# Kernel optimization log

Hardware: AMD Instinct MI355X
Metric: run time of the kernel (lower is better)

The kernel has to match this reference:

```python
import jax, jax.numpy as jnp
import numpy as np

N = 100_000      # nodes
E = 3_200_000    # edges (avg degree 32)
IN = 128         # input feature dim
H1, C1 = 8, 8    # layer-1 heads, channels per head (concat -> 64)
OUT = 2          # output classes (layer-2: 1 head, mean/no-concat)
NEG = 0.2        # LeakyReLU negative slope (PyG default)


def setup_inputs() -> dict:
    key = jax.random.key(0)
    ks = jax.random.split(key, 11)
    s1 = 1.0 / np.sqrt(IN)
    s2 = 1.0 / np.sqrt(H1 * C1)
    return {
        "x": jax.random.normal(ks[0], (N, IN), jnp.float32),
        "edge_index": jax.random.randint(ks[1], (2, E), 0, N, dtype=jnp.int32),
        "edge_attr": jax.random.normal(ks[2], (E, 1), jnp.float32),
        "W1": jax.random.normal(ks[3], (IN, H1 * C1), jnp.float32) * s1,
        "a1_src": jax.random.normal(ks[4], (H1, C1), jnp.float32) * s1,
        "a1_dst": jax.random.normal(ks[5], (H1, C1), jnp.float32) * s1,
        "b1": jnp.zeros((H1 * C1,), jnp.float32),
        "W2": jax.random.normal(ks[6], (H1 * C1, OUT), jnp.float32) * s2,
        "a2_src": jax.random.normal(ks[7], (1, OUT), jnp.float32) * s2,
        "a2_dst": jax.random.normal(ks[8], (1, OUT), jnp.float32) * s2,
        "b2": jnp.zeros((OUT,), jnp.float32),
    }


def gat_conv(x, W, a_src, a_dst, b, src, dst, heads, ch, concat):
    """PyG GATConv: per-head linear, per-edge LeakyReLU attention, segment softmax over dst."""
    n = x.shape[0]
    h = (x @ W).reshape(n, heads, ch)                 # [N, H, C]
    al_src = jnp.sum(h * a_src, axis=-1)              # [N, H]
    al_dst = jnp.sum(h * a_dst, axis=-1)              # [N, H]
    e = al_src[src] + al_dst[dst]                     # [Etot, H]
    e = jnp.where(e > 0, e, NEG * e)                  # LeakyReLU
    m = jax.lax.stop_gradient(jax.ops.segment_max(e, dst, num_segments=n))
    ex = jnp.exp(e - m[dst])
    den = jax.ops.segment_sum(ex, dst, num_segments=n)
    alpha = ex / den[dst]                             # segment softmax
    out = jax.ops.segment_sum(alpha[:, :, None] * h[src], dst, num_segments=n)  # [N, H, C]
    out = out.reshape(n, heads * ch) if concat else out.mean(axis=1)
    return out + b


def reference(x, edge_index, edge_attr, W1, a1_src, a1_dst, b1, W2, a2_src, a2_dst, b2):
    # add_self_loops=True (PyG default)
    loops = jnp.arange(x.shape[0], dtype=edge_index.dtype)
    src = jnp.concatenate([edge_index[0], loops])
    dst = jnp.concatenate([edge_index[1], loops])
    h = gat_conv(x, W1, a1_src, a1_dst, b1, src, dst, H1, C1, True)
    h = jax.nn.elu(h)
    return gat_conv(h, W2, a2_src, a2_dst, b2, src, dst, 1, OUT, False)
```

## Files before the change

kernel.cpp:

```cpp
#include <hip/hip_runtime.h>
#include <math.h>

#define NNODES 100000
#define NEDGES 3200000
#define ETOT   (NEDGES + NNODES)
#define IN_DIM 128
#define NH1    8
#define NC1    8
#define HC     64
#define OUTC   2
#define NEGSL  0.2f
#define L2E    1.44269504f

#define NBUCK 391
#define EPB   4096
#define NBLK  782
#define TOTC  (NBUCK * NBLK)


__global__ __launch_bounds__(256) void histA(const int* __restrict__ ei,
                                             int* __restrict__ carr) {
    __shared__ int lh[NBUCK];
    int tid = threadIdx.x;
    for (int i = tid; i < NBUCK; i += 256) lh[i] = 0;
    __syncthreads();
    const int* dptr = ei + NEDGES;
    int base = blockIdx.x * EPB;
#pragma unroll
    for (int i = 0; i < EPB / 1024; i++) {
        int idx = base + i * 1024 + tid * 4;
        if (idx < NEDGES) {
            int4 d4 = *(const int4*)&dptr[idx];
            atomicAdd(&lh[d4.x >> 8], 1);
            atomicAdd(&lh[d4.y >> 8], 1);
            atomicAdd(&lh[d4.z >> 8], 1);
            atomicAdd(&lh[d4.w >> 8], 1);
        }
    }
    __syncthreads();
    for (int i = tid; i < NBUCK; i += 256)
        carr[i * NBLK + blockIdx.x] = lh[i];
}

__global__ __launch_bounds__(256) void scanA(int* __restrict__ carr,
                                             int* __restrict__ bsums) {
    int gid = blockIdx.x * 256 + threadIdx.x;
    int v = (gid < TOTC) ? carr[gid] : 0;
    int lane = threadIdx.x & 63, w = threadIdx.x >> 6;
    int x = v;
    for (int off = 1; off < 64; off <<= 1) {
        int y = __shfl_up(x, off, 64);
        if (lane >= off) x += y;
    }
    __shared__ int wt[4];
    if (lane == 63) wt[w] = x;
    __syncthreads();
    int add = 0;
    for (int i = 0; i < w; i++) add += wt[i];
    int incl = x + add;
    if (gid < TOTC) carr[gid] = incl - v;
    if (threadIdx.x == 255) bsums[blockIdx.x] = incl;
}

__global__ __launch_bounds__(1024) void scanB(int* __restrict__ bsums, int nb) {
    int tid = threadIdx.x;
    int base = tid * 4;
    int v[4]; int tot = 0;
#pragma unroll
    for (int j = 0; j < 4; j++) {
        v[j] = (base + j < nb) ? bsums[base + j] : 0;
        tot += v[j];
    }
    int lane = tid & 63, w = tid >> 6;
    int x = tot;
    for (int off = 1; off < 64; off <<= 1) {
        int y = __shfl_up(x, off, 64);
        if (lane >= off) x += y;
    }
    __shared__ int wt[16];
    if (lane == 63) wt[w] = x;
    __syncthreads();
    int add = 0;
    for (int i = 0; i < w; i++) add += wt[i];
    int pre = x + add - tot;
#pragma unroll
    for (int j = 0; j < 4; j++) {
        if (base + j < nb) bsums[base + j] = pre;
        pre += v[j];
    }
}

__global__ __launch_bounds__(256) void scanC(int* __restrict__ carr,
                                             const int* __restrict__ bsums) {
    int gid = blockIdx.x * 256 + threadIdx.x;
    if (gid < TOTC) carr[gid] += bsums[gid >> 8];
}

__global__ __launch_bounds__(256) void scatC(const int* __restrict__ ei,
                                             const int* __restrict__ soff,
                                             int* __restrict__ ebuf) {
    __shared__ int soffL[NBUCK];
    __shared__ int lh[NBUCK];
    int tid = threadIdx.x;
    for (int i = tid; i < NBUCK; i += 256) {
        soffL[i] = soff[i * NBLK + blockIdx.x];
        lh[i] = 0;
    }
    __syncthreads();
    int base = blockIdx.x * EPB;
#pragma unroll
    for (int i = 0; i < EPB / 1024; i++) {
        int idx = base + i * 1024 + tid * 4;
        if (idx < NEDGES) {
            int4 s4 = *(const int4*)&ei[idx];
            int4 d4 = *(const int4*)&ei[NEDGES + idx];
            int b0 = d4.x >> 8, b1 = d4.y >> 8, b2 = d4.z >> 8, b3 = d4.w >> 8;
            int r0 = atomicAdd(&lh[b0], 1);
            int r1 = atomicAdd(&lh[b1], 1);
            int r2 = atomicAdd(&lh[b2], 1);
            int r3 = atomicAdd(&lh[b3], 1);
            ebuf[soffL[b0] + r0] = s4.x | ((d4.x & 255) << 17);
            ebuf[soffL[b1] + r1] = s4.y | ((d4.y & 255) << 17);
            ebuf[soffL[b2] + r2] = s4.z | ((d4.z & 255) << 17);
            ebuf[soffL[b3] + r3] = s4.w | ((d4.w & 255) << 17);
        }
    }
}

__global__ __launch_bounds__(256) void buildD(const int* __restrict__ soff,
                                              const int* __restrict__ ebuf,
                                              int* __restrict__ rowoff,
                                              int* __restrict__ srcs) {
    int b = blockIdx.x, tid = threadIdx.x;
    int nb = min(256, NNODES - b * 256);
    int ebeg = soff[b * NBLK];
    int eend = (b == NBUCK - 1) ? NEDGES : soff[(b + 1) * NBLK];
    __shared__ int cnt2[256];
    __shared__ int rowL[256];
    __shared__ int wsum[4];
    cnt2[tid] = 0;
    __syncthreads();
    for (int e = ebeg + tid; e < eend; e += 256)
        atomicAdd(&cnt2[(ebuf[e] >> 17) & 255], 1);
    __syncthreads();
    int v = (tid < nb) ? cnt2[tid] + 1 : 0;
    int lane = tid & 63, w = tid >> 6;
    int x = v;
    for (int off = 1; off < 64; off <<= 1) {
        int y = __shfl_up(x, off, 64);
        if (lane >= off) x += y;
    }
    if (lane == 63) wsum[w] = x;
    __syncthreads();
    int add = 0;
    for (int i = 0; i < w; i++) add += wsum[i];
    int fbase = ebeg + b * 256;
    int row = fbase + x + add - v;
    if (tid < nb) {
        rowL[tid] = row;
        int gnode = b * 256 + tid;
        rowoff[gnode] = row;
        srcs[row + cnt2[tid]] = gnode;
        if (gnode == NNODES - 1) rowoff[NNODES] = ETOT;
    }
    __syncthreads();
    cnt2[tid] = 0;
    __syncthreads();
    for (int e = ebeg + tid; e < eend; e += 256) {
        int wv = ebuf[e];
        int dl = (wv >> 17) & 255;
        int r = atomicAdd(&cnt2[dl], 1);
        srcs[rowL[dl] + r] = wv & 0x1FFFF;
    }
}


__global__ __launch_bounds__(256) void gemm1(const float* __restrict__ x,
                                             const float* __restrict__ W1,
                                             const float* __restrict__ a1s,
                                             const float* __restrict__ a1d,
                                             unsigned short* __restrict__ h1b,
                                             float2* __restrict__ alE,
                                             float* __restrict__ al1d) {
    __shared__ float sW[IN_DIM * HC];
    int tid = threadIdx.x;
    const float4* W4 = (const float4*)W1;
    float4* sW4 = (float4*)sW;
#pragma unroll
    for (int i = 0; i < 8; i++)
        sW4[tid + i * 256] = W4[tid + i * 256];
    __syncthreads();

    int w = __builtin_amdgcn_readfirstlane(tid >> 6);
    int lane = tid & 63;
    int node0 = blockIdx.x * 16 + w * 4;
    const float* xr = x + (size_t)node0 * IN_DIM;

    float acc0 = 0.f, acc1 = 0.f, acc2 = 0.f, acc3 = 0.f;
#pragma unroll 8
    for (int k = 0; k < IN_DIM; k++) {
        float wv = sW[k * HC + lane];
        acc0 = fmaf(xr[k], wv, acc0);
        acc1 = fmaf(xr[IN_DIM + k], wv, acc1);
        acc2 = fmaf(xr[2 * IN_DIM + k], wv, acc2);
        acc3 = fmaf(xr[3 * IN_DIM + k], wv, acc3);
    }

    float accs[4] = {acc0, acc1, acc2, acc3};
    int head = lane >> 3, c = lane & 7;
    float as = a1s[head * NC1 + c], adv = a1d[head * NC1 + c];
#pragma unroll
    for (int n = 0; n < 4; n++) {
        int node = node0 + n;
        unsigned int u = __float_as_uint(accs[n]);
        h1b[node * HC + lane] =
            (unsigned short)((u + 0x7FFF + ((u >> 16) & 1)) >> 16);
        float ps = accs[n] * as;
        float pd = accs[n] * adv;
        for (int off = 1; off < 8; off <<= 1) {
            ps += __shfl_xor(ps, off, 64);
            pd += __shfl_xor(pd, off, 64);
        }
        if (c == 0) {
            alE[node * NH1 + head] = make_float2(exp2f(ps * L2E),
                                                 exp2f(ps * (NEGSL * L2E)));
            al1d[node * NH1 + head] = pd;
        }
    }
}


__global__ __launch_bounds__(256) void agg1(const unsigned short* __restrict__ h1b,
                                            const float2* __restrict__ alE,
                                            const float* __restrict__ al1d,
                                            const float* __restrict__ b1,
                                            const float* __restrict__ W2,
                                            const float* __restrict__ a2s,
                                            const float* __restrict__ a2d,
                                            const int* __restrict__ rowoff,
                                            const int* __restrict__ srcs,
                                            float4* __restrict__ nd2,
                                            float* __restrict__ al2d) {
    int w = threadIdx.x >> 6, lane = threadIdx.x & 63;
    int node = blockIdx.x * 4 + w;
    int q = lane & 15;
    float ald = al1d[node * NH1 + (q & 7)];
    float E1d = exp2f(ald * L2E);
    float E2d = exp2f(ald * (NEGSL * L2E));
    int beg = __builtin_amdgcn_readfirstlane(rowoff[node]);
    int end = __builtin_amdgcn_readfirstlane(rowoff[node + 1]);
    int pidx = (lane & 0x30) | (q >> 1);

    float den = 0.f, a0 = 0.f, a1 = 0.f, a2 = 0.f, a3 = 0.f;
    for (int base = beg; base < end; base += 64) {
        int idx = base + lane;
        int sv = srcs[idx < end ? idx : end - 1];
        int nq = min(16, (end - base + 3) >> 2);
        for (int t = 0; t < nq; t++) {
            int s = __shfl(sv, 4 * t + (lane >> 4), 64);
            float p = 0.f;
            if (q < 8) {
                float2 ea = alE[s * NH1 + q];
                p = fmaxf(ea.x * E1d, ea.y * E2d);
            }
            p = __shfl(p, pidx, 64);
            bool valid = (base + 4 * t + (lane >> 4)) < end;
            p = valid ? p : 0.f;
            uint2 hv = *(const uint2*)&h1b[s * HC + 4 * q];
            den += p;
            a0 = fmaf(p, __uint_as_float(hv.x << 16), a0);
            a1 = fmaf(p, __uint_as_float(hv.x & 0xFFFF0000u), a1);
            a2 = fmaf(p, __uint_as_float(hv.y << 16), a2);
            a3 = fmaf(p, __uint_as_float(hv.y & 0xFFFF0000u), a3);
        }
    }
    den += __shfl_xor(den, 16, 64);  den += __shfl_xor(den, 32, 64);
    a0  += __shfl_xor(a0, 16, 64);   a0  += __shfl_xor(a0, 32, 64);
    a1  += __shfl_xor(a1, 16, 64);   a1  += __shfl_xor(a1, 32, 64);
    a2  += __shfl_xor(a2, 16, 64);   a2  += __shfl_xor(a2, 32, 64);
    a3  += __shfl_xor(a3, 16, 64);   a3  += __shfl_xor(a3, 32, 64);

    float rd = 1.f / den;
    float4 b1v = *(const float4*)&b1[4 * q];
    float o0 = fmaf(a0, rd, b1v.x);
    float o1 = fmaf(a1, rd, b1v.y);
    float o2 = fmaf(a2, rd, b1v.z);
    float o3 = fmaf(a3, rd, b1v.w);
    o0 = (o0 > 0.f) ? o0 : expm1f(o0);
    o1 = (o1 > 0.f) ? o1 : expm1f(o1);
    o2 = (o2 > 0.f) ? o2 : expm1f(o2);
    o3 = (o3 > 0.f) ? o3 : expm1f(o3);
    float4 w2a = *(const float4*)&W2[8 * q];
    float4 w2b = *(const float4*)&W2[8 * q + 4];
    float p0 = o0 * w2a.x + o1 * w2a.z + o2 * w2b.x + o3 * w2b.z;
    float p1 = o0 * w2a.y + o1 * w2a.w + o2 * w2b.y + o3 * w2b.w;
    for (int off = 1; off < 16; off <<= 1) {
        p0 += __shfl_xor(p0, off, 64);
        p1 += __shfl_xor(p1, off, 64);
    }
    if (lane == 0) {
        float l2s = p0 * a2s[0] + p1 * a2s[1];
        float l2d = p0 * a2d[0] + p1 * a2d[1];
        nd2[node] = make_float4(exp2f(l2s * L2E), exp2f(l2s * (NEGSL * L2E)),
                                p0, p1);
        al2d[node] = l2d;
    }
}


__global__ __launch_bounds__(256) void agg2(const float4* __restrict__ nd2,
                                            const float* __restrict__ al2d,
                                            const float* __restrict__ b2,
                                            const int* __restrict__ rowoff,
                                            const int* __restrict__ srcs,
                                            float* __restrict__ out) {
    int w = threadIdx.x >> 6, lane = threadIdx.x & 63;
    int n = blockIdx.x * 4 + w;
    if (n >= NNODES) return;
    float ald = al2d[n];
    float E1d = exp2f(ald * L2E);
    float E2d = exp2f(ald * (NEGSL * L2E));
    int beg = rowoff[n], end = rowoff[n + 1];
    float den = 0.f, a0 = 0.f, a1 = 0.f;
    for (int idx = beg + lane; idx < end; idx += 64) {
        int s = srcs[idx];
        float4 nd = nd2[s];
        float p = fmaxf(nd.x * E1d, nd.y * E2d);
        den += p;
        a0 = fmaf(p, nd.z, a0);
        a1 = fmaf(p, nd.w, a1);
    }
    for (int off = 1; off < 64; off <<= 1) {
        den += __shfl_xor(den, off, 64);
        a0  += __shfl_xor(a0, off, 64);
        a1  += __shfl_xor(a1, off, 64);
    }
    if (lane == 0) {
        out[n * 2 + 0] = a0 / den + b2[0];
        out[n * 2 + 1] = a1 / den + b2[1];
    }
}


extern "C" void kernel_launch(void* const* d_in, const int* in_sizes, int n_in,
                              void* d_out, int out_size, void* d_ws, size_t ws_size,
                              hipStream_t stream) {
    const float* x   = (const float*)d_in[0];
    const int*   ei  = (const int*)  d_in[1];
    const float* W1  = (const float*)d_in[3];
    const float* a1s = (const float*)d_in[4];
    const float* a1d = (const float*)d_in[5];
    const float* b1  = (const float*)d_in[6];
    const float* W2  = (const float*)d_in[7];
    const float* a2s = (const float*)d_in[8];
    const float* a2d = (const float*)d_in[9];
    const float* b2  = (const float*)d_in[10];
    float* out = (float*)d_out;

    char* ws = (char*)d_ws;
    unsigned short* h1b = (unsigned short*)ws;
    float2* alE   = (float2*)(ws + (size_t)NNODES * HC * 2);
    float* al1d_  = (float*)(alE + (size_t)NNODES * NH1);
    float4* nd2   = (float4*)(al1d_ + (size_t)NNODES * NH1);
    float* al2d_  = (float*)(nd2 + NNODES);
    int* rowoff   = (int*)(al2d_ + NNODES);
    int* srcs     = rowoff + NNODES + 1;
    int* ebuf     = (int*)ws;
    int* carr     = ebuf + NEDGES;
    int* bsums    = carr + TOTC;

    const int NB_SC  = (TOTC + 255) / 256;
    const int NB_N4  = (NNODES + 3) / 4;
    const int NB_G   = NNODES / 16;

    histA<<<NBLK, 256, 0, stream>>>(ei, carr);
    scanA<<<NB_SC, 256, 0, stream>>>(carr, bsums);
    scanB<<<1, 1024, 0, stream>>>(bsums, NB_SC);
    scanC<<<NB_SC, 256, 0, stream>>>(carr, bsums);
    scatC<<<NBLK, 256, 0, stream>>>(ei, carr, ebuf);
    buildD<<<NBUCK, 256, 0, stream>>>(carr, ebuf, rowoff, srcs);

    gemm1<<<NB_G, 256, 0, stream>>>(x, W1, a1s, a1d, h1b, alE, al1d_);

    agg1<<<NB_N4, 256, 0, stream>>>(h1b, alE, al1d_, b1, W2, a2s, a2d,
                                    rowoff, srcs, nd2, al2d_);

    agg2<<<NB_N4, 256, 0, stream>>>(nd2, al2d_, b2, rowoff, srcs, out);
}
```

Measured before the change: 273.6 us.

## Split layer-1 aggregation per head with head-major feature layout and partial reduction

```diff
diff --git a/kernel.cpp b/kernel.cpp
--- a/kernel.cpp
+++ b/kernel.cpp
@@ -179,8 +179,8 @@
                                              const float* __restrict__ W1,
                                              const float* __restrict__ a1s,
                                              const float* __restrict__ a1d,
-                                             unsigned short* __restrict__ h1b,
-                                             float2* __restrict__ alE,
+                                             unsigned short* __restrict__ h1e,
+                                             float2* __restrict__ alEq,
                                              float* __restrict__ al1d) {
     __shared__ float sW[IN_DIM * HC];
     int tid = threadIdx.x;
@@ -213,7 +213,7 @@
     for (int n = 0; n < 4; n++) {
         int node = node0 + n;
         unsigned int u = __float_as_uint(accs[n]);
-        h1b[node * HC + lane] =
+        h1e[((size_t)head * NNODES + node) * 8 + c] =
             (unsigned short)((u + 0x7FFF + ((u >> 16) & 1)) >> 16);
         float ps = accs[n] * as;
         float pd = accs[n] * adv;
@@ -222,89 +222,86 @@
             pd += __shfl_xor(pd, off, 64);
         }
         if (c == 0) {
-            alE[node * NH1 + head] = make_float2(exp2f(ps * L2E),
-                                                 exp2f(ps * (NEGSL * L2E)));
+            alEq[(size_t)head * NNODES + node] =
+                make_float2(exp2f(ps * L2E), exp2f(ps * (NEGSL * L2E)));
             al1d[node * NH1 + head] = pd;
         }
     }
 }
 
 
-__global__ __launch_bounds__(256) void agg1(const unsigned short* __restrict__ h1b,
-                                            const float2* __restrict__ alE,
-                                            const float* __restrict__ al1d,
-                                            const float* __restrict__ b1,
-                                            const float* __restrict__ W2,
-                                            const float* __restrict__ a2s,
-                                            const float* __restrict__ a2d,
-                                            const int* __restrict__ rowoff,
-                                            const int* __restrict__ srcs,
-                                            float4* __restrict__ nd2,
-                                            float* __restrict__ al2d) {
+__global__ __launch_bounds__(256) void agg1e(const unsigned short* __restrict__ h1e,
+                                             const float2* __restrict__ alEq,
+                                             const float* __restrict__ al1d,
+                                             const float* __restrict__ b1,
+                                             const float* __restrict__ W2,
+                                             const int* __restrict__ rowoff,
+                                             const int* __restrict__ srcs,
+                                             float2* __restrict__ part) {
+    int q = blockIdx.x & 7;
     int w = threadIdx.x >> 6, lane = threadIdx.x & 63;
-    int node = blockIdx.x * 4 + w;
-    int q = lane & 15;
-    float ald = al1d[node * NH1 + (q & 7)];
+    int node = (blockIdx.x >> 3) * 4 + w;
+    int e = lane >> 2, c = lane & 3;
+    const unsigned short* hrow = h1e + (size_t)q * NNODES * 8;
+    const float2* alp = alEq + (size_t)q * NNODES;
+    float ald = al1d[node * NH1 + q];
     float E1d = exp2f(ald * L2E);
     float E2d = exp2f(ald * (NEGSL * L2E));
     int beg = __builtin_amdgcn_readfirstlane(rowoff[node]);
     int end = __builtin_amdgcn_readfirstlane(rowoff[node + 1]);
-    int pidx = (lane & 0x30) | (q >> 1);
-
-    float den = 0.f, a0 = 0.f, a1 = 0.f, a2 = 0.f, a3 = 0.f;
-    for (int base = beg; base < end; base += 64) {
-        int idx = base + lane;
-        int sv = srcs[idx < end ? idx : end - 1];
-        int nq = min(16, (end - base + 3) >> 2);
-        for (int t = 0; t < nq; t++) {
-            int s = __shfl(sv, 4 * t + (lane >> 4), 64);
-            float p = 0.f;
-            if (q < 8) {
-                float2 ea = alE[s * NH1 + q];
-                p = fmaxf(ea.x * E1d, ea.y * E2d);
-            }
-            p = __shfl(p, pidx, 64);
-            bool valid = (base + 4 * t + (lane >> 4)) < end;
-            p = valid ? p : 0.f;
-            uint2 hv = *(const uint2*)&h1b[s * HC + 4 * q];
-            den += p;
-            a0 = fmaf(p, __uint_as_float(hv.x << 16), a0);
-            a1 = fmaf(p, __uint_as_float(hv.x & 0xFFFF0000u), a1);
-            a2 = fmaf(p, __uint_as_float(hv.y << 16), a2);
-            a3 = fmaf(p, __uint_as_float(hv.y & 0xFFFF0000u), a3);
-        }
-    }
-    den += __shfl_xor(den, 16, 64);  den += __shfl_xor(den, 32, 64);
-    a0  += __shfl_xor(a0, 16, 64);   a0  += __shfl_xor(a0, 32, 64);
-    a1  += __shfl_xor(a1, 16, 64);   a1  += __shfl_xor(a1, 32, 64);
-    a2  += __shfl_xor(a2, 16, 64);   a2  += __shfl_xor(a2, 32, 64);
-    a3  += __shfl_xor(a3, 16, 64);   a3  += __shfl_xor(a3, 32, 64);
+
+    float den = 0.f, acc0 = 0.f, acc1 = 0.f;
+    for (int i = beg; i < end; i += 16) {
+        int idx = i + e;
+        bool valid = idx < end;
+        int s = srcs[valid ? idx : end - 1];
+        float2 ea = alp[s];
+        unsigned int hv = *(const unsigned int*)&hrow[s * 8 + 2 * c];
+        float p = fmaxf(ea.x * E1d, ea.y * E2d);
+        p = valid ? p : 0.f;
+        den += p;
+        acc0 = fmaf(p, __uint_as_float(hv << 16), acc0);
+        acc1 = fmaf(p, __uint_as_float(hv & 0xFFFF0000u), acc1);
+    }
+    den  += __shfl_xor(den, 4, 64);   den  += __shfl_xor(den, 8, 64);
+    den  += __shfl_xor(den, 16, 64);  den  += __shfl_xor(den, 32, 64);
+    acc0 += __shfl_xor(acc0, 4, 64);  acc0 += __shfl_xor(acc0, 8, 64);
+    acc0 += __shfl_xor(acc0, 16, 64); acc0 += __shfl_xor(acc0, 32, 64);
+    acc1 += __shfl_xor(acc1, 4, 64);  acc1 += __shfl_xor(acc1, 8, 64);
+    acc1 += __shfl_xor(acc1, 16, 64); acc1 += __shfl_xor(acc1, 32, 64);
 
     float rd = 1.f / den;
-    float4 b1v = *(const float4*)&b1[4 * q];
-    float o0 = fmaf(a0, rd, b1v.x);
-    float o1 = fmaf(a1, rd, b1v.y);
-    float o2 = fmaf(a2, rd, b1v.z);
-    float o3 = fmaf(a3, rd, b1v.w);
+    int ch = 8 * q + 2 * c;
+    float2 b1v = *(const float2*)&b1[ch];
+    float o0 = fmaf(acc0, rd, b1v.x);
+    float o1 = fmaf(acc1, rd, b1v.y);
     o0 = (o0 > 0.f) ? o0 : expm1f(o0);
     o1 = (o1 > 0.f) ? o1 : expm1f(o1);
-    o2 = (o2 > 0.f) ? o2 : expm1f(o2);
-    o3 = (o3 > 0.f) ? o3 : expm1f(o3);
-    float4 w2a = *(const float4*)&W2[8 * q];
-    float4 w2b = *(const float4*)&W2[8 * q + 4];
-    float p0 = o0 * w2a.x + o1 * w2a.z + o2 * w2b.x + o3 * w2b.z;
-    float p1 = o0 * w2a.y + o1 * w2a.w + o2 * w2b.y + o3 * w2b.w;
-    for (int off = 1; off < 16; off <<= 1) {
-        p0 += __shfl_xor(p0, off, 64);
-        p1 += __shfl_xor(p1, off, 64);
-    }
-    if (lane == 0) {
-        float l2s = p0 * a2s[0] + p1 * a2s[1];
-        float l2d = p0 * a2d[0] + p1 * a2d[1];
-        nd2[node] = make_float4(exp2f(l2s * L2E), exp2f(l2s * (NEGSL * L2E)),
-                                p0, p1);
-        al2d[node] = l2d;
-    }
+    float4 w2v = *(const float4*)&W2[2 * ch];
+    float p0 = o0 * w2v.x + o1 * w2v.z;
+    float p1 = o0 * w2v.y + o1 * w2v.w;
+    p0 += __shfl_xor(p0, 1, 64);  p0 += __shfl_xor(p0, 2, 64);
+    p1 += __shfl_xor(p1, 1, 64);  p1 += __shfl_xor(p1, 2, 64);
+    if (lane == 0) part[(size_t)q * NNODES + node] = make_float2(p0, p1);
+}
+
+__global__ __launch_bounds__(256) void fin1(const float2* __restrict__ part,
+                                            const float* __restrict__ a2s,
+                                            const float* __restrict__ a2d,
+                                            float4* __restrict__ nd2,
+                                            float* __restrict__ al2d) {
+    int n = blockIdx.x * 256 + threadIdx.x;
+    if (n >= NNODES) return;
+    float s0 = 0.f, s1 = 0.f;
+#pragma unroll
+    for (int q = 0; q < 8; q++) {
+        float2 pp = part[(size_t)q * NNODES + n];
+        s0 += pp.x; s1 += pp.y;
+    }
+    float l2s = s0 * a2s[0] + s1 * a2s[1];
+    float l2d = s0 * a2d[0] + s1 * a2d[1];
+    nd2[n] = make_float4(exp2f(l2s * L2E), exp2f(l2s * (NEGSL * L2E)), s0, s1);
+    al2d[n] = l2d;
 }
 
 
@@ -358,18 +355,20 @@
     float* out = (float*)d_out;
 
     char* ws = (char*)d_ws;
-    unsigned short* h1b = (unsigned short*)ws;
-    float2* alE   = (float2*)(ws + (size_t)NNODES * HC * 2);
-    float* al1d_  = (float*)(alE + (size_t)NNODES * NH1);
+    unsigned short* h1e = (unsigned short*)ws;
+    float2* alEq  = (float2*)(ws + (size_t)NNODES * HC * 2);
+    float* al1d_  = (float*)(alEq + (size_t)NNODES * NH1);
     float4* nd2   = (float4*)(al1d_ + (size_t)NNODES * NH1);
     float* al2d_  = (float*)(nd2 + NNODES);
     int* rowoff   = (int*)(al2d_ + NNODES);
     int* srcs     = rowoff + NNODES + 1;
+    float2* part  = (float2*)(srcs + ETOT);
     int* ebuf     = (int*)ws;
     int* carr     = ebuf + NEDGES;
     int* bsums    = carr + TOTC;
 
     const int NB_SC  = (TOTC + 255) / 256;
+    const int NB_N   = (NNODES + 255) / 256;
     const int NB_N4  = (NNODES + 3) / 4;
     const int NB_G   = NNODES / 16;
 
@@ -380,10 +379,11 @@
     scatC<<<NBLK, 256, 0, stream>>>(ei, carr, ebuf);
     buildD<<<NBUCK, 256, 0, stream>>>(carr, ebuf, rowoff, srcs);
 
-    gemm1<<<NB_G, 256, 0, stream>>>(x, W1, a1s, a1d, h1b, alE, al1d_);
-
-    agg1<<<NB_N4, 256, 0, stream>>>(h1b, alE, al1d_, b1, W2, a2s, a2d,
-                                    rowoff, srcs, nd2, al2d_);
+    gemm1<<<NB_G, 256, 0, stream>>>(x, W1, a1s, a1d, h1e, alEq, al1d_);
+
+    agg1e<<<8 * NB_N4, 256, 0, stream>>>(h1e, alEq, al1d_, b1, W2,
+                                         rowoff, srcs, part);
+    fin1<<<NB_N, 256, 0, stream>>>(part, a2s, a2d, nd2, al2d_);
 
     agg2<<<NB_N4, 256, 0, stream>>>(nd2, al2d_, b2, rowoff, srcs, out);
 }
```

After: 473.4 us. 1.73x slower.
